# Kernel optimization log

Measured on AMD Instinct MI355X. Metric: run time of the kernel, lower is better.

Reference implementation:

```python
import jax, jax.numpy as jnp
import numpy as np

NH = 8          # number of attention heads
RAND_P = 0.1    # random attention probability
EPS = 1e-5      # LayerNorm eps (torch default)


def _layer_norm(x, g, b):
    m = x.mean(-1, keepdims=True)
    v = ((x - m) ** 2).mean(-1, keepdims=True)
    return (x - m) * jax.lax.rsqrt(v + EPS) * g + b


def _make_mask(u, n_frames, spatial):
    # random(0/1) + tiled-eye position mask + block-diagonal frame mask (additive float mask)
    L = n_frames * spatial
    idx = jnp.arange(L)
    frame_id = idx // spatial
    pos_id = idx % spatial
    rand = (u >= RAND_P).astype(jnp.float32)
    pos = (pos_id[:, None] == pos_id[None, :]).astype(jnp.float32)
    frame = (frame_id[:, None] == frame_id[None, :]).astype(jnp.float32)
    return rand + pos + frame  # [L, L], values in {0,1,2,3}


def _attn_block(f, u, Wqkv, bqkv, Wo, bo, g1, b1, Wfc1, bfc1, Wfc2, bfc2, g2, b2):
    N, C, H, W = f.shape
    S = H * W
    L = N * S
    hd = C // NH
    src = f.transpose(0, 2, 3, 1).reshape(L, C)  # (n,h,w) flatten order, batch=1 squeezed
    mask = _make_mask(u, N, S)

    qkv = src @ Wqkv.T + bqkv                    # [L, 3C]
    q, k, v = jnp.split(qkv, 3, axis=-1)
    q = q.reshape(L, NH, hd).transpose(1, 0, 2) * (hd ** -0.5)  # [H, L, hd]
    k = k.reshape(L, NH, hd).transpose(1, 0, 2)
    v = v.reshape(L, NH, hd).transpose(1, 0, 2)

    scores = jnp.einsum('hqd,hkd->hqk', q, k) + mask[None]      # [H, L, L]
    attn = jax.nn.softmax(scores, axis=-1)
    o = jnp.einsum('hqk,hkd->hqd', attn, v).transpose(1, 0, 2).reshape(L, C)
    src2 = o @ Wo.T + bo

    x = _layer_norm(src + src2, g1, b1)          # residual + LN (dropout p=0 -> identity)
    h = jax.nn.relu(x @ Wfc1.T + bfc1)
    x = _layer_norm(x + h @ Wfc2.T + bfc2, g2, b2)
    return x.reshape(N, H, W, C).transpose(0, 3, 1, 2)


def setup_inputs() -> dict:
    key = jax.random.key(0)
    ks = jax.random.split(key, 12)
    D = 256
    s = 0.02
    return {
        'f0': jax.random.normal(ks[0], (2, D, 80, 80), jnp.float32),
        'f1': jax.random.normal(ks[1], (2, D, 40, 40), jnp.float32),
        'f2': jax.random.normal(ks[2], (2, D, 32, 32), jnp.float32),
        'f3': jax.random.normal(ks[3], (2, D, 16, 16), jnp.float32),
        'u2': jax.random.uniform(ks[4], (2048, 2048), jnp.float32),
        'u3': jax.random.uniform(ks[5], (512, 512), jnp.float32),
        'Wqkv': jax.random.normal(ks[6], (3 * D, D), jnp.float32) * s,
        'bqkv': jnp.zeros((3 * D,), jnp.float32),
        'Wo': jax.random.normal(ks[7], (D, D), jnp.float32) * s,
        'bo': jnp.zeros((D,), jnp.float32),
        'g1': jnp.ones((D,), jnp.float32),
        'b1': jnp.zeros((D,), jnp.float32),
        'Wfc1': jax.random.normal(ks[8], (4 * D, D), jnp.float32) * s,
        'bfc1': jnp.zeros((4 * D,), jnp.float32),
        'Wfc2': jax.random.normal(ks[9], (D, 4 * D), jnp.float32) * s,
        'bfc2': jnp.zeros((D,), jnp.float32),
        'g2': jnp.ones((D,), jnp.float32),
        'b2': jnp.zeros((D,), jnp.float32),
    }


def reference(f0, f1, f2, f3, u2, u3, Wqkv, bqkv, Wo, bo, g1, b1,
              Wfc1, bfc1, Wfc2, bfc2, g2, b2):
    params = (Wqkv, bqkv, Wo, bo, g1, b1, Wfc1, bfc1, Wfc2, bfc2, g2, b2)
    # levels 0 and 1 pass through untouched (loop starts at i=2)
    out2 = _attn_block(f2, u2, *params)
    out3 = _attn_block(f3, u3, *params)
    return (f0, f1, out2, out3)
```

## Files before the change

kernel.cpp:

```cpp
#include <hip/hip_runtime.h>
#include <hip/hip_bf16.h>
#include <cstddef>
#include <cmath>


typedef __attribute__((ext_vector_type(8))) short s16x8;
typedef __attribute__((ext_vector_type(4))) short s16x4;
typedef __attribute__((ext_vector_type(4))) float f32x4;
typedef __attribute__((ext_vector_type(2))) unsigned int u32x2;
typedef unsigned short ushort_t;
typedef unsigned long long u64;

#define RTOT 2560
#define HIPL 69632
#define LOG2E 1.4426950408889634f

__device__ inline unsigned short f2bf(float x) {
    union { __hip_bfloat16 h; unsigned short u; } cv;
    cv.h = __float2bfloat16(x);
    return cv.u;
}
__device__ inline float bf2f(unsigned short u) {
    union { unsigned int i; float f; } cv;
    cv.i = ((unsigned int)u) << 16;
    return cv.f;
}
__device__ inline float fexp2(float x) { return exp2f(x); }

__global__ __launch_bounds__(256) void prep(const float* __restrict__ wqkv,
                                            const float* __restrict__ wo,
                                            const float* __restrict__ wfc1,
                                            const float* __restrict__ wfc2,
                                            ushort_t* __restrict__ o1,
                                            ushort_t* __restrict__ o2,
                                            ushort_t* __restrict__ o3,
                                            ushort_t* __restrict__ o4,
                                            const float* __restrict__ u2,
                                            const float* __restrict__ u3,
                                            u64* __restrict__ ub,
                                            const float* __restrict__ f2,
                                            const float* __restrict__ f3,
                                            ushort_t* __restrict__ srcb) {
    __shared__ float tl[64][65];
    int bid = blockIdx.x;
    int t = threadIdx.x;
    if (bid < 160) {
        int b = bid;
        const float* src; int S, rowb, n, ct, ht;
        if (b < 128) {
            n = b >> 6; int rem = b & 63; ct = rem >> 4; ht = rem & 15;
            src = f2; S = 1024; rowb = 0;
        } else {
            int b2 = b - 128;
            n = b2 >> 4; int rem = b2 & 15; ct = rem >> 2; ht = rem & 3;
            src = f3; S = 256; rowb = 2048;
        }
        int c0 = ct * 64, hw0 = ht * 64;
        int i = t >> 6, lane = t & 63;
#pragma unroll
        for (int jj = 0; jj < 16; ++jj) {
            int cl = i * 16 + jj;
            tl[lane][cl] = src[(size_t)(n * 256 + c0 + cl) * S + hw0 + lane];
        }
        __syncthreads();
#pragma unroll
        for (int jj = 0; jj < 16; ++jj) {
            int hl = i * 16 + jj;
            int row = rowb + n * S + hw0 + hl;
            srcb[(size_t)row * 256 + c0 + lane] = f2bf(tl[hl][lane]);
        }
    } else if (bid < 928) {
        int i = (bid - 160) * 256 + t;
        const float* src; ushort_t* dst; int li;
        if (i < 49152)       { src = wqkv; dst = o1; li = i; }
        else if (i < 65536)  { src = wo;   dst = o2; li = i - 49152; }
        else if (i < 131072) { src = wfc1; dst = o3; li = i - 65536; }
        else                 { src = wfc2; dst = o4; li = i - 131072; }
        f32x4 v = ((const f32x4*)src)[li];
        s16x4 r;
        r[0] = (short)f2bf(v[0]); r[1] = (short)f2bf(v[1]);
        r[2] = (short)f2bf(v[2]); r[3] = (short)f2bf(v[3]);
        ((s16x4*)dst)[li] = r;
    } else {
        int gw = ((bid - 928) * 256 + t) >> 6;
        int lane = t & 63;
        const float* p;
        u64* dstLo;
        int q, kb, smask, sshift;
        if (gw < 16384) {
            int row = gw >> 3, ch = gw & 7;
            p = &u2[(size_t)row * 2048 + ch * 256 + lane * 4];
            dstLo = &ub[(size_t)gw * 4];
            q = row; kb = ch * 256 + lane * 4; smask = 1023; sshift = 10;
        } else {
            int lw = gw - 16384;
            int row = lw >> 1, ch = lw & 1;
            p = &u3[(size_t)row * 512 + ch * 256 + lane * 4];
            dstLo = &ub[65536 + (size_t)lw * 4];
            q = row; kb = ch * 256 + lane * 4; smask = 255; sshift = 8;
        }
        u64* dstHi = dstLo + HIPL;
        f32x4 v = *(const f32x4*)p;
        int qp = q & smask, qf = q >> sshift;
        u64 bl[4], bh[4];
#pragma unroll
        for (int j = 0; j < 4; ++j) {
            int k = kb + j;
            int val = (v[j] >= 0.1f ? 1 : 0)
                    + ((k & smask) == qp ? 1 : 0)
                    + ((k >> sshift) == qf ? 1 : 0);
            bl[j] = __ballot((val & 1) != 0);
            bh[j] = __ballot((val & 2) != 0);
        }
        if (lane < 4) {
            u64 x = (lane == 0) ? bl[0] : (lane == 1) ? bl[1]
                  : (lane == 2) ? bl[2] : bl[3];
            dstLo[lane] = x;
        } else if (lane < 8) {
            int j = lane - 4;
            u64 x = (j == 0) ? bh[0] : (j == 1) ? bh[1]
                  : (j == 2) ? bh[2] : bh[3];
            dstHi[j] = x;
        }
    }
}

#define ASTR 72

template <int EPI>
__global__ __launch_bounds__(256) void gemm64(const ushort_t* __restrict__ A,
                                              const ushort_t* __restrict__ W,
                                              const float* __restrict__ bias,
                                              ushort_t* __restrict__ outb,
                                              int M, int N, int K) {
    __shared__ __align__(16) ushort_t As[2][64 * ASTR];
    __shared__ __align__(16) ushort_t Ws[2][64 * ASTR];

    const int t = threadIdx.x;
    const int w = t >> 6, l = t & 63;
    const int c = l & 15, g = l >> 4;
    const int mh = w >> 1, nh = w & 1;
    const int m0 = blockIdx.y * 64, n0 = blockIdx.x * 64;
    const int srow = t >> 3;
    const int cg8 = (t & 7) * 8;

    const ushort_t* Aip0 = &A[(size_t)(m0 + srow) * K + cg8];
    const ushort_t* Aip1 = &A[(size_t)(m0 + 32 + srow) * K + cg8];
    const ushort_t* Wip0 = &W[(size_t)(n0 + srow) * K + cg8];
    const ushort_t* Wip1 = &W[(size_t)(n0 + 32 + srow) * K + cg8];

    s16x8 ra0 = *(const s16x8*)Aip0;
    s16x8 ra1 = *(const s16x8*)Aip1;
    s16x8 rw0 = *(const s16x8*)Wip0;
    s16x8 rw1 = *(const s16x8*)Wip1;
    *(s16x8*)&As[0][srow * ASTR + cg8] = ra0;
    *(s16x8*)&As[0][(32 + srow) * ASTR + cg8] = ra1;
    *(s16x8*)&Ws[0][srow * ASTR + cg8] = rw0;
    *(s16x8*)&Ws[0][(32 + srow) * ASTR + cg8] = rw1;
    __syncthreads();

    f32x4 acc[2][2] = {{{0.f,0.f,0.f,0.f},{0.f,0.f,0.f,0.f}},
                       {{0.f,0.f,0.f,0.f},{0.f,0.f,0.f,0.f}}};
    const int nsteps = K >> 6;

    for (int ks = 0; ks < nsteps; ++ks) {
        const int b = ks & 1;
        const bool pf = (ks + 1 < nsteps);
        if (pf) {
            int ko = (ks + 1) << 6;
            ra0 = *(const s16x8*)(Aip0 + ko);
            ra1 = *(const s16x8*)(Aip1 + ko);
            rw0 = *(const s16x8*)(Wip0 + ko);
            rw1 = *(const s16x8*)(Wip1 + ko);
        }
#pragma unroll
        for (int sl = 0; sl < 2; ++sl) {
            s16x8 af0 = *(const s16x8*)&As[b][(32 * mh + c) * ASTR + sl * 32 + 8 * g];
            s16x8 af1 = *(const s16x8*)&As[b][(32 * mh + 16 + c) * ASTR + sl * 32 + 8 * g];
            s16x8 wf0 = *(const s16x8*)&Ws[b][(32 * nh + c) * ASTR + sl * 32 + 8 * g];
            s16x8 wf1 = *(const s16x8*)&Ws[b][(32 * nh + 16 + c) * ASTR + sl * 32 + 8 * g];
            acc[0][0] = __builtin_amdgcn_mfma_f32_16x16x32_bf16(af0, wf0, acc[0][0], 0, 0, 0);
            acc[0][1] = __builtin_amdgcn_mfma_f32_16x16x32_bf16(af0, wf1, acc[0][1], 0, 0, 0);
            acc[1][0] = __builtin_amdgcn_mfma_f32_16x16x32_bf16(af1, wf0, acc[1][0], 0, 0, 0);
            acc[1][1] = __builtin_amdgcn_mfma_f32_16x16x32_bf16(af1, wf1, acc[1][1], 0, 0, 0);
        }
        if (pf) {
            int nb = b ^ 1;
            *(s16x8*)&As[nb][srow * ASTR + cg8] = ra0;
            *(s16x8*)&As[nb][(32 + srow) * ASTR + cg8] = ra1;
            *(s16x8*)&Ws[nb][srow * ASTR + cg8] = rw0;
            *(s16x8*)&Ws[nb][(32 + srow) * ASTR + cg8] = rw1;
        }
        __syncthreads();
    }

#pragma unroll
    for (int i = 0; i < 2; ++i)
#pragma unroll
    for (int j = 0; j < 2; ++j) {
        int n = n0 + 32 * nh + 16 * j + c;
        float bv = bias[n];
        float sc = 1.f;
        if (EPI == 3) sc = (n < 256) ? 0.17677669529663687f * LOG2E : 1.f;
#pragma unroll
        for (int r = 0; r < 4; ++r) {
            int m = m0 + 32 * mh + 16 * i + 4 * g + r;
            float v = acc[i][j][r] + bv;
            if (EPI == 1) v = fmaxf(v, 0.f);
            if (EPI == 3) v *= sc;
            outb[(size_t)m * N + n] = f2bf(v);
        }
    }
}

__global__ __launch_bounds__(128) void gemm_fc2(const ushort_t* __restrict__ A,
                                                const ushort_t* __restrict__ W,
                                                const float* __restrict__ bias,
                                                const ushort_t* __restrict__ res,
                                                ushort_t* __restrict__ outb,
                                                int M, int N, int K) {
    __shared__ __align__(16) ushort_t As[2][32 * ASTR];
    __shared__ __align__(16) ushort_t Ws[2][32 * ASTR];

    const int t = threadIdx.x;
    const int w = t >> 6, l = t & 63;
    const int c = l & 15, g = l >> 4;
    const int m0 = blockIdx.y * 32, n0 = blockIdx.x * 32;
    const int srow = t >> 3;
    const int cg8 = (t & 7) * 8;

    const ushort_t* Aip0 = &A[(size_t)(m0 + srow) * K + cg8];
    const ushort_t* Aip1 = &A[(size_t)(m0 + 16 + srow) * K + cg8];
    const ushort_t* Wip0 = &W[(size_t)(n0 + srow) * K + cg8];
    const ushort_t* Wip1 = &W[(size_t)(n0 + 16 + srow) * K + cg8];

    s16x8 ra0 = *(const s16x8*)Aip0;
    s16x8 ra1 = *(const s16x8*)Aip1;
    s16x8 rw0 = *(const s16x8*)Wip0;
    s16x8 rw1 = *(const s16x8*)Wip1;
    *(s16x8*)&As[0][srow * ASTR + cg8] = ra0;
    *(s16x8*)&As[0][(16 + srow) * ASTR + cg8] = ra1;
    *(s16x8*)&Ws[0][srow * ASTR + cg8] = rw0;
    *(s16x8*)&Ws[0][(16 + srow) * ASTR + cg8] = rw1;
    __syncthreads();

    f32x4 acc[2] = {{0.f, 0.f, 0.f, 0.f}, {0.f, 0.f, 0.f, 0.f}};
    const int nsteps = K >> 6;

    for (int ks = 0; ks < nsteps; ++ks) {
        const int b = ks & 1;
        const bool pf = (ks + 1 < nsteps);
        if (pf) {
            int ko = (ks + 1) << 6;
            ra0 = *(const s16x8*)(Aip0 + ko);
            ra1 = *(const s16x8*)(Aip1 + ko);
            rw0 = *(const s16x8*)(Wip0 + ko);
            rw1 = *(const s16x8*)(Wip1 + ko);
        }
#pragma unroll
        for (int kt = 0; kt < 2; ++kt) {
            s16x8 af = *(const s16x8*)&As[b][(16 * w + c) * ASTR + kt * 32 + 8 * g];
            s16x8 wf0 = *(const s16x8*)&Ws[b][c * ASTR + kt * 32 + 8 * g];
            s16x8 wf1 = *(const s16x8*)&Ws[b][(16 + c) * ASTR + kt * 32 + 8 * g];
            acc[0] = __builtin_amdgcn_mfma_f32_16x16x32_bf16(af, wf0, acc[0], 0, 0, 0);
            acc[1] = __builtin_amdgcn_mfma_f32_16x16x32_bf16(af, wf1, acc[1], 0, 0, 0);
        }
        if (pf) {
            int nb = b ^ 1;
            *(s16x8*)&As[nb][srow * ASTR + cg8] = ra0;
            *(s16x8*)&As[nb][(16 + srow) * ASTR + cg8] = ra1;
            *(s16x8*)&Ws[nb][srow * ASTR + cg8] = rw0;
            *(s16x8*)&Ws[nb][(16 + srow) * ASTR + cg8] = rw1;
        }
        __syncthreads();
    }

#pragma unroll
    for (int nt = 0; nt < 2; ++nt) {
        int n = n0 + 16 * nt + c;
        float bv = bias[n];
#pragma unroll
        for (int r = 0; r < 4; ++r) {
            int m = m0 + 16 * w + 4 * g + r;
            float v = acc[nt][r] + bv + bf2f(res[(size_t)m * N + n]);
            outb[(size_t)m * N + n] = f2bf(v);
        }
    }
}

__global__ __launch_bounds__(128) void gemm_wo(const ushort_t* __restrict__ Opart,
                                               const float2* __restrict__ ml,
                                               const ushort_t* __restrict__ W,
                                               const float* __restrict__ bias,
                                               const ushort_t* __restrict__ res,
                                               ushort_t* __restrict__ outb) {
    const int K = 256, N = 256;
    __shared__ __align__(16) ushort_t As[2][32 * ASTR];
    __shared__ __align__(16) ushort_t Ws[2][32 * ASTR];

    const int t = threadIdx.x;
    const int w = t >> 6, l = t & 63;
    const int c = l & 15, g = l >> 4;
    const int m0 = blockIdx.y * 32, n0 = blockIdx.x * 32;
    const int srow = t >> 3;
    const int cg8 = (t & 7) * 8;

    auto loadA = [&](int row, int kcol) -> s16x8 {
        int head = kcol >> 5;
        float2 a0 = ml[((size_t)0 * RTOT + row) * 8 + head];
        float2 a1 = ml[((size_t)1 * RTOT + row) * 8 + head];
        float2 a2 = ml[((size_t)2 * RTOT + row) * 8 + head];
        float2 a3 = ml[((size_t)3 * RTOT + row) * 8 + head];
        float M = fmaxf(fmaxf(a0.x, a1.x), fmaxf(a2.x, a3.x));
        float w1 = fexp2(a0.x - M), w2 = fexp2(a1.x - M);
        float w3 = fexp2(a2.x - M), w4 = fexp2(a3.x - M);
        float inv = 1.f / (w1 * a0.y + w2 * a1.y + w3 * a2.y + w4 * a3.y);
        const size_t str = (size_t)RTOT * 256;
        size_t base = (size_t)row * 256 + kcol;
        s16x8 o1 = *(const s16x8*)&Opart[base];
        s16x8 o2 = *(const s16x8*)&Opart[base + str];
        s16x8 o3 = *(const s16x8*)&Opart[base + 2 * str];
        s16x8 o4 = *(const s16x8*)&Opart[base + 3 * str];
        s16x8 r;
#pragma unroll
        for (int e = 0; e < 8; ++e) {
            float v = w1 * bf2f((ushort_t)o1[e]) + w2 * bf2f((ushort_t)o2[e])
                    + w3 * bf2f((ushort_t)o3[e]) + w4 * bf2f((ushort_t)o4[e]);
            r[e] = (short)f2bf(v * inv);
        }
        return r;
    };

    const ushort_t* Wip0 = &W[(size_t)(n0 + srow) * K + cg8];
    const ushort_t* Wip1 = &W[(size_t)(n0 + 16 + srow) * K + cg8];

    s16x8 ra0 = loadA(m0 + srow, cg8);
    s16x8 ra1 = loadA(m0 + 16 + srow, cg8);
    s16x8 rw0 = *(const s16x8*)Wip0;
    s16x8 rw1 = *(const s16x8*)Wip1;
    *(s16x8*)&As[0][srow * ASTR + cg8] = ra0;
    *(s16x8*)&As[0][(16 + srow) * ASTR + cg8] = ra1;
    *(s16x8*)&Ws[0][srow * ASTR + cg8] = rw0;
    *(s16x8*)&Ws[0][(16 + srow) * ASTR + cg8] = rw1;
    __syncthreads();

    f32x4 acc[2] = {{0.f, 0.f, 0.f, 0.f}, {0.f, 0.f, 0.f, 0.f}};
    const int nsteps = 4;

    for (int ks = 0; ks < nsteps; ++ks) {
        const int b = ks & 1;
        const bool pf = (ks + 1 < nsteps);
        if (pf) {
            int ko = (ks + 1) << 6;
            ra0 = loadA(m0 + srow, ko + cg8);
            ra1 = loadA(m0 + 16 + srow, ko + cg8);
            rw0 = *(const s16x8*)(Wip0 + ko);
            rw1 = *(const s16x8*)(Wip1 + ko);
        }
#pragma unroll
        for (int kt = 0; kt < 2; ++kt) {
            s16x8 af = *(const s16x8*)&As[b][(16 * w + c) * ASTR + kt * 32 + 8 * g];
            s16x8 wf0 = *(const s16x8*)&Ws[b][c * ASTR + kt * 32 + 8 * g];
            s16x8 wf1 = *(const s16x8*)&Ws[b][(16 + c) * ASTR + kt * 32 + 8 * g];
            acc[0] = __builtin_amdgcn_mfma_f32_16x16x32_bf16(af, wf0, acc[0], 0, 0, 0);
            acc[1] = __builtin_amdgcn_mfma_f32_16x16x32_bf16(af, wf1, acc[1], 0, 0, 0);
        }
        if (pf) {
            int nb = b ^ 1;
            *(s16x8*)&As[nb][srow * ASTR + cg8] = ra0;
            *(s16x8*)&As[nb][(16 + srow) * ASTR + cg8] = ra1;
            *(s16x8*)&Ws[nb][srow * ASTR + cg8] = rw0;
            *(s16x8*)&Ws[nb][(16 + srow) * ASTR + cg8] = rw1;
        }
        __syncthreads();
    }

#pragma unroll
    for (int nt = 0; nt < 2; ++nt) {
        int n = n0 + 16 * nt + c;
        float bv = bias[n];
#pragma unroll
        for (int r = 0; r < 4; ++r) {
            int m = m0 + 16 * w + 4 * g + r;
            float v = acc[nt][r] + bv + bf2f(res[(size_t)m * 256 + n]);
            outb[(size_t)m * 256 + n] = f2bf(v);
        }
    }
}

#define KS 40
#define VS 66
#define PS 72
#define OS 68

__global__ __launch_bounds__(256) void flash_split(const ushort_t* __restrict__ qkvb,
                                                   const u64* __restrict__ ubits,
                                                   ushort_t* __restrict__ Opart,
                                                   float2* __restrict__ ml,
                                                   const float* __restrict__ f0,
                                                   const float* __restrict__ f1,
                                                   float* __restrict__ outp) {
    __shared__ __align__(16) ushort_t ks[2][64 * KS];
    __shared__ __align__(16) ushort_t vts[2][32 * VS];
    __shared__ __align__(16) char pso[64 * PS * 2];
    ushort_t* ps = (ushort_t*)pso;
    float* os = (float*)pso;

    const int bx = blockIdx.x;
    const int t = threadIdx.x;

    if (bx >= 1280) {
        int idx = (bx - 1280) * 256 + t;
        f32x4 v = (idx < 819200) ? ((const f32x4*)f0)[idx]
                                 : ((const f32x4*)f1)[idx - 819200];
        ((f32x4*)outp)[idx] = v;
        return;
    }

    int qt, h, split, L, rowbase;
    const u64* ub;
    if (bx < 1024) {
        qt = bx & 31; h = (bx >> 5) & 7; split = bx >> 8;
        L = 2048; rowbase = 0; ub = ubits;
    } else {
        int lo = bx - 1024;
        qt = lo & 7; h = (lo >> 3) & 7; split = lo >> 6;
        L = 512; rowbase = 2048; ub = ubits + 65536;
    }
    const int tps = (L >> 6) >> 2;
    const int ts0 = split * tps;
    const int nch = L >> 8;

    const int w = t >> 6;
    const int l = t & 63;
    const int c = l & 15;
    const int g = l >> 4;

    const int srow = t >> 2;
    const int sc8 = (t & 3) * 8;
    const int q0g = rowbase + qt * 64;

    const int ql = qt * 64 + 16 * w + c;
    const s16x8 qf = *(const s16x8*)&qkvb[(size_t)(rowbase + ql) * 768 + h * 32 + 8 * g];
    const u64* ubq = &ub[(size_t)ql * nch * 4];

    s16x8 kreg, vreg;
    {
        size_t base = (size_t)(rowbase + ts0 * 64 + srow) * 768 + h * 32 + sc8;
        s16x8 k0r = *(const s16x8*)&qkvb[base + 256];
        s16x8 v0r = *(const s16x8*)&qkvb[base + 512];
        *(s16x8*)&ks[0][srow * KS + sc8] = k0r;
#pragma unroll
        for (int i = 0; i < 8; ++i)
            vts[0][(sc8 + i) * VS + srow] = (ushort_t)v0r[i];
        if (tps > 1) {
            kreg = *(const s16x8*)&qkvb[base + 64 * 768 + 256];
            vreg = *(const s16x8*)&qkvb[base + 64 * 768 + 512];
        }
    }
    __syncthreads();

    f32x4 oacc0 = {0.f, 0.f, 0.f, 0.f};
    f32x4 oacc1 = {0.f, 0.f, 0.f, 0.f};
    float mold = -3e38f;
    float lsum = 0.f;
    const f32x4 zc = {0.f, 0.f, 0.f, 0.f};

    u64 wl0 = 0, wl1 = 0, wl2 = 0, wl3 = 0;
    u64 wh0 = 0, wh1 = 0, wh2 = 0, wh3 = 0;
    int cur = 0;
    for (int kt = 0; kt < tps; ++kt) {
        const int nxt = cur ^ 1;
        const int gt = ts0 + kt;

        if (kt + 1 < tps) {
            *(s16x8*)&ks[nxt][srow * KS + sc8] = kreg;
#pragma unroll
            for (int i = 0; i < 8; ++i)
                vts[nxt][(sc8 + i) * VS + srow] = (ushort_t)vreg[i];
        }
        if (kt + 2 < tps) {
            size_t base = (size_t)(rowbase + (gt + 2) * 64 + srow) * 768 + h * 32 + sc8;
            kreg = *(const s16x8*)&qkvb[base + 256];
            vreg = *(const s16x8*)&qkvb[base + 512];
        }

        if ((gt & 3) == 0 || kt == 0) {
            const u64* bp = &ubq[(size_t)(gt >> 2) * 4];
            wl0 = bp[0]; wl1 = bp[1]; wl2 = bp[2]; wl3 = bp[3];
            wh0 = bp[HIPL]; wh1 = bp[HIPL + 1]; wh2 = bp[HIPL + 2]; wh3 = bp[HIPL + 3];
        }
        const unsigned shb = 16 * (gt & 3);

        f32x4 sacc[4];
        __builtin_amdgcn_s_setprio(1);
#pragma unroll
        for (int nt = 0; nt < 4; ++nt) {
            s16x8 kf = *(const s16x8*)&ks[cur][(16 * nt + c) * KS + 8 * g];
            sacc[nt] = __builtin_amdgcn_mfma_f32_16x16x32_bf16(kf, qf, zc, 0, 0, 0);
        }
        __builtin_amdgcn_s_setprio(0);

        float sv[4][4];
        float pmax = -3e38f;
#pragma unroll
        for (int nt = 0; nt < 4; ++nt) {
            unsigned sh = shb + 4 * nt + g;
#pragma unroll
            for (int r = 0; r < 4; ++r) {
                u64 wl = (r == 0) ? wl0 : (r == 1) ? wl1 : (r == 2) ? wl2 : wl3;
                u64 wh = (r == 0) ? wh0 : (r == 1) ? wh1 : (r == 2) ? wh2 : wh3;
                unsigned lo = (unsigned)(wl >> sh) & 1u;
                unsigned hi = (unsigned)(wh >> sh) & 1u;
                float s = fmaf((float)(lo + 2u * hi), LOG2E, sacc[nt][r]);
                sv[nt][r] = s;
                pmax = fmaxf(pmax, s);
            }
        }
        if (!__all(pmax <= mold + 11.5415f)) {
            float m = pmax;
            m = fmaxf(m, __shfl_xor(m, 16));
            m = fmaxf(m, __shfl_xor(m, 32));
            float newm = fmaxf(mold, m);
            float fac = fexp2(mold - newm);
            mold = newm;
            lsum *= fac;
            oacc0 *= fac;
            oacc1 *= fac;
        }

        float sum = 0.f;
#pragma unroll
        for (int nt = 0; nt < 4; ++nt) {
            float p0 = fexp2(sv[nt][0] - mold);
            float p1 = fexp2(sv[nt][1] - mold);
            float p2 = fexp2(sv[nt][2] - mold);
            float p3 = fexp2(sv[nt][3] - mold);
            sum += (p0 + p1) + (p2 + p3);
            u32x2 pk;
            pk[0] = ((unsigned)f2bf(p1) << 16) | f2bf(p0);
            pk[1] = ((unsigned)f2bf(p3) << 16) | f2bf(p2);
            *(u32x2*)&ps[(16 * w + c) * PS + 16 * nt + 4 * g] = pk;
        }
        lsum += sum;

        __builtin_amdgcn_s_setprio(1);
#pragma unroll
        for (int kc = 0; kc < 2; ++kc) {
            s16x8 pfr = *(const s16x8*)&ps[(16 * w + c) * PS + 32 * kc + 8 * g];
            s16x8 vf0 = *(const s16x8*)&vts[cur][c * VS + 32 * kc + 8 * g];
            s16x8 vf1 = *(const s16x8*)&vts[cur][(16 + c) * VS + 32 * kc + 8 * g];
            oacc0 = __builtin_amdgcn_mfma_f32_16x16x32_bf16(vf0, pfr, oacc0, 0, 0, 0);
            oacc1 = __builtin_amdgcn_mfma_f32_16x16x32_bf16(vf1, pfr, oacc1, 0, 0, 0);
        }
        __builtin_amdgcn_s_setprio(0);

        __syncthreads();
        cur = nxt;
    }

    float lrun = lsum;
    lrun += __shfl_xor(lrun, 16);
    lrun += __shfl_xor(lrun, 32);

    if (g == 0) {
        int q = q0g + 16 * w + c;
        ml[((size_t)split * RTOT + q) * 8 + h] = make_float2(mold, lrun);
    }

#pragma unroll
    for (int r = 0; r < 4; ++r) {
        os[(4 * g + r) * OS + 16 * w + c] = oacc0[r];
        os[(16 + 4 * g + r) * OS + 16 * w + c] = oacc1[r];
    }
    __syncthreads();
    {
        int r = t >> 2, d0 = (t & 3) * 8;
        s16x8 pk;
#pragma unroll
        for (int i = 0; i < 8; ++i) pk[i] = (short)f2bf(os[(d0 + i) * OS + r]);
        *(s16x8*)&Opart[((size_t)split * RTOT + q0g + r) * 256 + h * 32 + d0] = pk;
    }
}

__global__ __launch_bounds__(256) void ln1_kernel(const ushort_t* __restrict__ in,
                                                  const float* __restrict__ g,
                                                  const float* __restrict__ b,
                                                  ushort_t* __restrict__ outb) {
    int t = threadIdx.x;
    int row = blockIdx.x * 4 + (t >> 6);
    int lane = t & 63;
    size_t base = (size_t)row * 256 + lane * 4;
    s16x4 x = *(const s16x4*)&in[base];
    float v[4];
    float s1 = 0.f, s2 = 0.f;
#pragma unroll
    for (int e = 0; e < 4; ++e) {
        v[e] = bf2f((ushort_t)x[e]);
        s1 += v[e];
        s2 += v[e] * v[e];
    }
#pragma unroll
    for (int d = 1; d < 64; d <<= 1) {
        s1 += __shfl_xor(s1, d);
        s2 += __shfl_xor(s2, d);
    }
    float mean = s1 * (1.f / 256.f);
    float var = s2 * (1.f / 256.f) - mean * mean;
    float rstd = rsqrtf(var + 1e-5f);
    s16x4 r;
#pragma unroll
    for (int e = 0; e < 4; ++e) {
        int n = lane * 4 + e;
        r[e] = (short)f2bf((v[e] - mean) * rstd * g[n] + b[n]);
    }
    *(s16x4*)&outb[base] = r;
}

__global__ __launch_bounds__(256) void ln2_stats(const ushort_t* __restrict__ in,
                                                 float2* __restrict__ stats) {
    int t = threadIdx.x;
    int row = blockIdx.x * 4 + (t >> 6);
    int lane = t & 63;
    s16x4 x = *(const s16x4*)&in[(size_t)row * 256 + lane * 4];
    float s1 = 0.f, s2 = 0.f;
#pragma unroll
    for (int e = 0; e < 4; ++e) {
        float v = bf2f((ushort_t)x[e]);
        s1 += v;
        s2 += v * v;
    }
#pragma unroll
    for (int d = 1; d < 64; d <<= 1) {
        s1 += __shfl_xor(s1, d);
        s2 += __shfl_xor(s2, d);
    }
    if (lane == 0) {
        float mean = s1 * (1.f / 256.f);
        float var = s2 * (1.f / 256.f) - mean * mean;
        stats[row] = make_float2(mean, rsqrtf(var + 1e-5f));
    }
}

__global__ __launch_bounds__(256) void ln2_scatter(const ushort_t* __restrict__ in,
                                                   const float2* __restrict__ stats,
                                                   const float* __restrict__ g,
                                                   const float* __restrict__ b,
                                                   float* __restrict__ out2,
                                                   float* __restrict__ out3) {
    __shared__ float tl[64][65];
    int bid = blockIdx.x;
    int t = threadIdx.x;
    float* dst; int S, rowb, n, ct, ht;
    if (bid < 128) {
        n = bid >> 6; int rem = bid & 63; ct = rem >> 4; ht = rem & 15;
        dst = out2; S = 1024; rowb = 0;
    } else {
        int b2 = bid - 128;
        n = b2 >> 4; int rem = b2 & 15; ct = rem >> 2; ht = rem & 3;
        dst = out3; S = 256; rowb = 2048;
    }
    int c0 = ct * 64, hw0 = ht * 64;
    int i = t >> 6, lane = t & 63;
    float gv = g[c0 + lane], bv = b[c0 + lane];
#pragma unroll
    for (int jj = 0; jj < 16; ++jj) {
        int hl = i * 16 + jj;
        int row = rowb + n * S + hw0 + hl;
        float2 st = stats[row];
        float v = bf2f(in[(size_t)row * 256 + c0 + lane]);
        tl[hl][lane] = (v - st.x) * st.y * gv + bv;
    }
    __syncthreads();
#pragma unroll
    for (int jj = 0; jj < 16; ++jj) {
        int cl = i * 16 + jj;
        dst[(size_t)(n * 256 + c0 + cl) * S + hw0 + lane] = tl[lane][cl];
    }
}


extern "C" void kernel_launch(void* const* d_in, const int* in_sizes, int n_in,
                              void* d_out, int out_size, void* d_ws, size_t ws_size,
                              hipStream_t stream) {
    const float* f0 = (const float*)d_in[0];
    const float* f1 = (const float*)d_in[1];
    const float* f2 = (const float*)d_in[2];
    const float* f3 = (const float*)d_in[3];
    const float* u2 = (const float*)d_in[4];
    const float* u3 = (const float*)d_in[5];
    const float* Wqkv = (const float*)d_in[6];
    const float* bqkv = (const float*)d_in[7];
    const float* Wo   = (const float*)d_in[8];
    const float* bo   = (const float*)d_in[9];
    const float* g1   = (const float*)d_in[10];
    const float* b1   = (const float*)d_in[11];
    const float* Wfc1 = (const float*)d_in[12];
    const float* bfc1 = (const float*)d_in[13];
    const float* Wfc2 = (const float*)d_in[14];
    const float* bfc2 = (const float*)d_in[15];
    const float* g2   = (const float*)d_in[16];
    const float* b2   = (const float*)d_in[17];

    float* out = (float*)d_out;
    float* ws = (float*)d_ws;

    ushort_t* wqkv = (ushort_t*)ws;
    ushort_t* wo   = (ushort_t*)(ws + 98304);
    ushort_t* wfc1 = (ushort_t*)(ws + 131072);
    ushort_t* wfc2 = (ushort_t*)(ws + 262144);

    float* sc = ws + 393216;
    ushort_t* src_bf = (ushort_t*)sc;
    ushort_t* qkvb   = (ushort_t*)(sc + 327680);
    ushort_t* t1b    = (ushort_t*)(sc + 1310720);
    ushort_t* x_bf   = (ushort_t*)(sc + 1638400);
    ushort_t* t2b    = (ushort_t*)(sc + 1966080);
    u64*      ubits  = (u64*)(sc + 2293760);
    float2*   ml     = (float2*)(sc + 2572288);
    float2*   st2    = (float2*)(sc + 2736128);
    ushort_t* Opart  = (ushort_t*)(sc + 2741248);
    ushort_t* h_bf   = Opart;

    prep<<<5280, 256, 0, stream>>>(Wqkv, Wo, Wfc1, Wfc2, wqkv, wo, wfc1, wfc2,
                                   u2, u3, ubits, f2, f3, src_bf);

    gemm64<3><<<dim3(12, 40), 256, 0, stream>>>(
        src_bf, wqkv, bqkv, qkvb, RTOT, 768, 256);
    flash_split<<<5280, 256, 0, stream>>>(qkvb, ubits, Opart, ml, f0, f1, out);
    gemm_wo<<<dim3(8, 80), 128, 0, stream>>>(Opart, ml, wo, bo, src_bf, t1b);
    ln1_kernel<<<640, 256, 0, stream>>>(t1b, g1, b1, x_bf);
    gemm64<1><<<dim3(16, 40), 256, 0, stream>>>(
        x_bf, wfc1, bfc1, h_bf, RTOT, 1024, 256);
    gemm_fc2<<<dim3(8, 80), 128, 0, stream>>>(
        h_bf, wfc2, bfc2, x_bf, t2b, RTOT, 256, 1024);
    ln2_stats<<<640, 256, 0, stream>>>(t2b, st2);
    ln2_scatter<<<160, 256, 0, stream>>>(t2b, st2, g2, b2,
                                         out + 4096000, out + 4620288);
}
```

Measured before the change: 78.80 us.

## Move mask bit-packing into QKV GEMM launch and retune flash LDS strides

```diff
diff --git a/kernel.cpp b/kernel.cpp
--- a/kernel.cpp
+++ b/kernel.cpp
@@ -35,9 +35,6 @@
                                             ushort_t* __restrict__ o2,
                                             ushort_t* __restrict__ o3,
                                             ushort_t* __restrict__ o4,
-                                            const float* __restrict__ u2,
-                                            const float* __restrict__ u3,
-                                            u64* __restrict__ ub,
                                             const float* __restrict__ f2,
                                             const float* __restrict__ f3,
                                             ushort_t* __restrict__ srcb) {
@@ -69,7 +66,7 @@
             int row = rowb + n * S + hw0 + hl;
             srcb[(size_t)row * 256 + c0 + lane] = f2bf(tl[hl][lane]);
         }
-    } else if (bid < 928) {
+    } else {
         int i = (bid - 160) * 256 + t;
         const float* src; ushort_t* dst; int li;
         if (i < 49152)       { src = wqkv; dst = o1; li = i; }
@@ -81,8 +78,23 @@
         r[0] = (short)f2bf(v[0]); r[1] = (short)f2bf(v[1]);
         r[2] = (short)f2bf(v[2]); r[3] = (short)f2bf(v[3]);
         ((s16x4*)dst)[li] = r;
-    } else {
-        int gw = ((bid - 928) * 256 + t) >> 6;
+    }
+}
+
+#define ASTR 72
+
+__global__ __launch_bounds__(256) void gemm_qkv(const ushort_t* __restrict__ A,
+                                                const ushort_t* __restrict__ W,
+                                                const float* __restrict__ bias,
+                                                ushort_t* __restrict__ outb,
+                                                const float* __restrict__ u2,
+                                                const float* __restrict__ u3,
+                                                u64* __restrict__ ub) {
+    const int bid = blockIdx.x;
+    const int t = threadIdx.x;
+
+    if (bid >= 480) {
+        int gw = ((bid - 480) * 256 + t) >> 6;
         int lane = t & 63;
         const float* p;
         u64* dstLo;
@@ -122,25 +134,17 @@
                   : (j == 2) ? bh[2] : bh[3];
             dstHi[j] = x;
         }
-    }
-}
-
-#define ASTR 72
-
-template <int EPI>
-__global__ __launch_bounds__(256) void gemm64(const ushort_t* __restrict__ A,
-                                              const ushort_t* __restrict__ W,
-                                              const float* __restrict__ bias,
-                                              ushort_t* __restrict__ outb,
-                                              int M, int N, int K) {
+        return;
+    }
+
+    const int N = 768, K = 256;
     __shared__ __align__(16) ushort_t As[2][64 * ASTR];
     __shared__ __align__(16) ushort_t Ws[2][64 * ASTR];
 
-    const int t = threadIdx.x;
     const int w = t >> 6, l = t & 63;
     const int c = l & 15, g = l >> 4;
     const int mh = w >> 1, nh = w & 1;
-    const int m0 = blockIdx.y * 64, n0 = blockIdx.x * 64;
+    const int m0 = (bid / 12) * 64, n0 = (bid % 12) * 64;
     const int srow = t >> 3;
     const int cg8 = (t & 7) * 8;
 
@@ -200,14 +204,92 @@
     for (int j = 0; j < 2; ++j) {
         int n = n0 + 32 * nh + 16 * j + c;
         float bv = bias[n];
-        float sc = 1.f;
-        if (EPI == 3) sc = (n < 256) ? 0.17677669529663687f * LOG2E : 1.f;
+        float sc = (n < 256) ? 0.17677669529663687f * LOG2E : 1.f;
 #pragma unroll
         for (int r = 0; r < 4; ++r) {
             int m = m0 + 32 * mh + 16 * i + 4 * g + r;
-            float v = acc[i][j][r] + bv;
-            if (EPI == 1) v = fmaxf(v, 0.f);
-            if (EPI == 3) v *= sc;
+            float v = (acc[i][j][r] + bv) * sc;
+            outb[(size_t)m * N + n] = f2bf(v);
+        }
+    }
+}
+
+__global__ __launch_bounds__(256) void gemm_fc1(const ushort_t* __restrict__ A,
+                                                const ushort_t* __restrict__ W,
+                                                const float* __restrict__ bias,
+                                                ushort_t* __restrict__ outb,
+                                                int M, int N, int K) {
+    __shared__ __align__(16) ushort_t As[2][64 * ASTR];
+    __shared__ __align__(16) ushort_t Ws[2][64 * ASTR];
+
+    const int t = threadIdx.x;
+    const int w = t >> 6, l = t & 63;
+    const int c = l & 15, g = l >> 4;
+    const int mh = w >> 1, nh = w & 1;
+    const int m0 = blockIdx.y * 64, n0 = blockIdx.x * 64;
+    const int srow = t >> 3;
+    const int cg8 = (t & 7) * 8;
+
+    const ushort_t* Aip0 = &A[(size_t)(m0 + srow) * K + cg8];
+    const ushort_t* Aip1 = &A[(size_t)(m0 + 32 + srow) * K + cg8];
+    const ushort_t* Wip0 = &W[(size_t)(n0 + srow) * K + cg8];
+    const ushort_t* Wip1 = &W[(size_t)(n0 + 32 + srow) * K + cg8];
+
+    s16x8 ra0 = *(const s16x8*)Aip0;
+    s16x8 ra1 = *(const s16x8*)Aip1;
+    s16x8 rw0 = *(const s16x8*)Wip0;
+    s16x8 rw1 = *(const s16x8*)Wip1;
+    *(s16x8*)&As[0][srow * ASTR + cg8] = ra0;
+    *(s16x8*)&As[0][(32 + srow) * ASTR + cg8] = ra1;
+    *(s16x8*)&Ws[0][srow * ASTR + cg8] = rw0;
+    *(s16x8*)&Ws[0][(32 + srow) * ASTR + cg8] = rw1;
+    __syncthreads();
+
+    f32x4 acc[2][2] = {{{0.f,0.f,0.f,0.f},{0.f,0.f,0.f,0.f}},
+                       {{0.f,0.f,0.f,0.f},{0.f,0.f,0.f,0.f}}};
+    const int nsteps = K >> 6;
+
+    for (int ks = 0; ks < nsteps; ++ks) {
+        const int b = ks & 1;
+        const bool pf = (ks + 1 < nsteps);
+        if (pf) {
+            int ko = (ks + 1) << 6;
+            ra0 = *(const s16x8*)(Aip0 + ko);
+            ra1 = *(const s16x8*)(Aip1 + ko);
+            rw0 = *(const s16x8*)(Wip0 + ko);
+            rw1 = *(const s16x8*)(Wip1 + ko);
+        }
+#pragma unroll
+        for (int sl = 0; sl < 2; ++sl) {
+            s16x8 af0 = *(const s16x8*)&As[b][(32 * mh + c) * ASTR + sl * 32 + 8 * g];
+            s16x8 af1 = *(const s16x8*)&As[b][(32 * mh + 16 + c) * ASTR + sl * 32 + 8 * g];
+            s16x8 wf0 = *(const s16x8*)&Ws[b][(32 * nh + c) * ASTR + sl * 32 + 8 * g];
+            s16x8 wf1 = *(const s16x8*)&Ws[b][(32 * nh + 16 + c) * ASTR + sl * 32 + 8 * g];
+            acc[0][0] = __builtin_amdgcn_mfma_f32_16x16x32_bf16(af0, wf0, acc[0][0], 0, 0, 0);
+            acc[0][1] = __builtin_amdgcn_mfma_f32_16x16x32_bf16(af0, wf1, acc[0][1], 0, 0, 0);
+            acc[1][0] = __builtin_amdgcn_mfma_f32_16x16x32_bf16(af1, wf0, acc[1][0], 0, 0, 0);
+            acc[1][1] = __builtin_amdgcn_mfma_f32_16x16x32_bf16(af1, wf1, acc[1][1], 0, 0, 0);
+        }
+        if (pf) {
+            int nb = b ^ 1;
+            *(s16x8*)&As[nb][srow * ASTR + cg8] = ra0;
+            *(s16x8*)&As[nb][(32 + srow) * ASTR + cg8] = ra1;
+            *(s16x8*)&Ws[nb][srow * ASTR + cg8] = rw0;
+            *(s16x8*)&Ws[nb][(32 + srow) * ASTR + cg8] = rw1;
+        }
+        __syncthreads();
+    }
+
+#pragma unroll
+    for (int i = 0; i < 2; ++i)
+#pragma unroll
+    for (int j = 0; j < 2; ++j) {
+        int n = n0 + 32 * nh + 16 * j + c;
+        float bv = bias[n];
+#pragma unroll
+        for (int r = 0; r < 4; ++r) {
+            int m = m0 + 32 * mh + 16 * i + 4 * g + r;
+            float v = fmaxf(acc[i][j][r] + bv, 0.f);
             outb[(size_t)m * N + n] = f2bf(v);
         }
     }
@@ -388,9 +470,9 @@
     }
 }
 
-#define KS 40
+#define KS 36
 #define VS 66
-#define PS 72
+#define PS 68
 #define OS 68
 
 __global__ __launch_bounds__(256) void flash_split(const ushort_t* __restrict__ qkvb,
@@ -722,15 +804,14 @@
     ushort_t* Opart  = (ushort_t*)(sc + 2741248);
     ushort_t* h_bf   = Opart;
 
-    prep<<<5280, 256, 0, stream>>>(Wqkv, Wo, Wfc1, Wfc2, wqkv, wo, wfc1, wfc2,
-                                   u2, u3, ubits, f2, f3, src_bf);
-
-    gemm64<3><<<dim3(12, 40), 256, 0, stream>>>(
-        src_bf, wqkv, bqkv, qkvb, RTOT, 768, 256);
+    prep<<<928, 256, 0, stream>>>(Wqkv, Wo, Wfc1, Wfc2, wqkv, wo, wfc1, wfc2,
+                                  f2, f3, src_bf);
+
+    gemm_qkv<<<4832, 256, 0, stream>>>(src_bf, wqkv, bqkv, qkvb, u2, u3, ubits);
     flash_split<<<5280, 256, 0, stream>>>(qkvb, ubits, Opart, ml, f0, f1, out);
     gemm_wo<<<dim3(8, 80), 128, 0, stream>>>(Opart, ml, wo, bo, src_bf, t1b);
     ln1_kernel<<<640, 256, 0, stream>>>(t1b, g1, b1, x_bf);
-    gemm64<1><<<dim3(16, 40), 256, 0, stream>>>(
+    gemm_fc1<<<dim3(16, 40), 256, 0, stream>>>(
         x_bf, wfc1, bfc1, h_bf, RTOT, 1024, 256);
     gemm_fc2<<<dim3(8, 80), 128, 0, stream>>>(
         h_bf, wfc2, bfc2, x_bf, t2b, RTOT, 256, 1024);
```

Result: slower. 84.15 us (+6.8%).
